# Kernel tuning notes

Measured on AMD Instinct MI355X. Metric: run time of the kernel, lower is better.

The kernel has to match this reference:

```python
import jax, jax.numpy as jnp
import numpy as np

N_SP, N_SPAT = 20000, 10000
E_SS, E_BIP, E_SP = 160000, 320000, 320000
H, C = 4, 64  # GAT heads / per-head channels (hidden_channels=64, concat=False)
EPS = 1e-6


def _gat(xs, xd, row, col, ea, Ws, Wd, a_s, a_d, a_e, We, b, num_dst, heads, ch, self_loops, concat):
    # PyG GATConv with edge_dim: linear -> per-head additive attention -> softmax over incoming edges -> scatter-add
    hs = (xs @ Ws).reshape(-1, heads, ch)          # [Ns,H,C]
    hd = (xd @ Wd).reshape(-1, heads, ch)          # [Nd,H,C]
    al_s = jnp.sum(hs * a_s, -1)                   # [Ns,H]
    al_d = jnp.sum(hd * a_d, -1)                   # [Nd,H]
    if self_loops:
        # add_self_loops with fill_value='mean': loop edge_attr = mean of incoming edge_attr per node
        cnt = jax.ops.segment_sum(jnp.ones((row.shape[0],), ea.dtype), col, num_dst)
        loop_ea = jax.ops.segment_sum(ea, col, num_dst) / jnp.maximum(cnt, 1.0)[:, None]
        loops = jnp.arange(num_dst, dtype=row.dtype)
        row = jnp.concatenate([row, loops])
        col = jnp.concatenate([col, loops])
        ea = jnp.concatenate([ea, loop_ea], 0)
    he = (ea @ We).reshape(-1, heads, ch)          # [E,H,C]
    al = jax.nn.leaky_relu(al_s[row] + al_d[col] + jnp.sum(he * a_e, -1), 0.2)  # [E,H]
    m = jax.ops.segment_max(al, col, num_segments=num_dst)
    ex = jnp.exp(al - m[col])
    den = jax.ops.segment_sum(ex, col, num_segments=num_dst)
    alpha = ex / (den[col] + 1e-16)
    out = jax.ops.segment_sum(hs[row] * alpha[..., None], col, num_segments=num_dst)  # [Nd,H,C]
    out = out.reshape(num_dst, heads * ch) if concat else out.mean(1)
    return out + b


def setup_inputs() -> dict:
    key = jax.random.key(0)
    ks = iter(jax.random.split(key, 64))
    f = lambda shape: jax.random.normal(next(ks), shape, jnp.float32)
    w = lambda shape: f(shape) / np.sqrt(shape[0])
    inp = {}
    inp['species_x_mean'] = f((N_SP, 32))
    inp['species_x_std'] = jax.random.uniform(next(ks), (N_SP, 32), jnp.float32)
    inp['traits_nanmask'] = jax.random.bernoulli(next(ks), 0.4, (N_SP, 32))
    inp['species_x_gen'] = f((N_SP, 64))
    inp['species_x_phylo'] = f((N_SP, 128))
    inp['spatial_x'] = f((N_SPAT, 12))
    inp['spatial_global_data'] = f((N_SPAT, 4))
    ei = lambda e, ns, nd: jnp.stack([jax.random.randint(next(ks), (e,), 0, ns, jnp.int32),
                                      jax.random.randint(next(ks), (e,), 0, nd, jnp.int32)])
    inp['ss_edge_index'] = ei(E_SS, N_SPAT, N_SPAT)
    inp['ss_edge_attr'] = jax.random.uniform(next(ks), (E_SS, 1), jnp.float32)
    inp['bip_edge_index'] = ei(E_BIP, N_SPAT, N_SP)
    inp['bip_edge_attr'] = jax.random.uniform(next(ks), (E_BIP, 1), jnp.float32)
    inp['sp_edge_index'] = ei(E_SP, N_SP, N_SP)
    inp['sp_edge_attr'] = jax.random.uniform(next(ks), (E_SP, 1), jnp.float32)
    # GAT conv params: space_gnn (sg0, sg1), species_gnn (pg0, pg1)
    for nm, din in [('sg0', 16), ('sg1', 64), ('pg0', 128), ('pg1', 64)]:
        inp[nm + '_W'] = w((din, H * C))
        inp[nm + '_as'] = f((H, C)) * 0.1
        inp[nm + '_ad'] = f((H, C)) * 0.1
        inp[nm + '_ae'] = f((H, C)) * 0.1
        inp[nm + '_We'] = w((1, H * C))
        inp[nm + '_b'] = jnp.zeros((C,), jnp.float32)
    # bipartite GATConv: heads=1, concat=True, src dim=hidden=64, dst dim=in_gen+in_phylo=192
    inp['bp_Ws'] = w((64, 64))
    inp['bp_Wd'] = w((192, 64))
    inp['bp_as'] = f((1, 64)) * 0.1
    inp['bp_ad'] = f((1, 64)) * 0.1
    inp['bp_ae'] = f((1, 64)) * 0.1
    inp['bp_We'] = w((1, 64))
    inp['bp_b'] = jnp.zeros((64,), jnp.float32)
    inp['sl_W'] = w((288, 64))
    inp['sl_b'] = jnp.zeros((64,), jnp.float32)
    inp['fc_W'] = w((64, 64))
    inp['fc_b'] = jnp.zeros((64,), jnp.float32)
    return inp


def reference(species_x_mean, species_x_std, traits_nanmask, species_x_gen, species_x_phylo,
              spatial_x, spatial_global_data, ss_edge_index, ss_edge_attr, bip_edge_index,
              bip_edge_attr, sp_edge_index, sp_edge_attr,
              sg0_W, sg0_as, sg0_ad, sg0_ae, sg0_We, sg0_b,
              sg1_W, sg1_as, sg1_ad, sg1_ae, sg1_We, sg1_b,
              pg0_W, pg0_as, pg0_ad, pg0_ae, pg0_We, pg0_b,
              pg1_W, pg1_as, pg1_ad, pg1_ae, pg1_We, pg1_b,
              bp_Ws, bp_Wd, bp_as, bp_ad, bp_ae, bp_We, bp_b,
              sl_W, sl_b, fc_W, fc_b):
    # inference path: no trait masking -> visibility = observed mask
    vis = (~traits_nanmask).astype(jnp.float32)
    sp_in = jnp.concatenate([species_x_mean, species_x_std, vis, species_x_gen, species_x_phylo], 1)
    sp_in = jax.nn.relu(sp_in @ sl_W + sl_b)                      # [N_SP,64]
    # spatial GNN (2 GATConv layers, heads=4, concat=False, self loops)
    h = jnp.concatenate([spatial_x, spatial_global_data], 1)      # [N_SPAT,16]
    r, c = ss_edge_index[0], ss_edge_index[1]
    h = jax.nn.relu(_gat(h, h, r, c, ss_edge_attr, sg0_W, sg0_W, sg0_as, sg0_ad, sg0_ae, sg0_We, sg0_b, N_SPAT, H, C, True, False))
    h = jax.nn.relu(_gat(h, h, r, c, ss_edge_attr, sg1_W, sg1_W, sg1_as, sg1_ad, sg1_ae, sg1_We, sg1_b, N_SPAT, H, C, True, False))
    # bipartite spatial->species GATConv (heads=1, concat=True, no self loops)
    part = jnp.concatenate([species_x_gen, species_x_phylo], 1)   # [N_SP,192]
    br, bc = bip_edge_index[0], bip_edge_index[1]
    sts = jax.nn.relu(_gat(h, part, br, bc, bip_edge_attr, bp_Ws, bp_Wd, bp_as, bp_ad, bp_ae, bp_We, bp_b, N_SP, 1, 64, False, True))
    # species GNN (2 GATConv layers)
    x = jnp.concatenate([sts, sp_in], 1)                          # [N_SP,128]
    pr, pc = sp_edge_index[0], sp_edge_index[1]
    x = jax.nn.relu(_gat(x, x, pr, pc, sp_edge_attr, pg0_W, pg0_W, pg0_as, pg0_ad, pg0_ae, pg0_We, pg0_b, N_SP, H, C, True, False))
    x = jax.nn.relu(_gat(x, x, pr, pc, sp_edge_attr, pg1_W, pg1_W, pg1_as, pg1_ad, pg1_ae, pg1_We, pg1_b, N_SP, H, C, True, False))
    ms = x @ fc_W + fc_b                                          # [N_SP, 2*out]
    mean, log_std = jnp.split(ms, 2, axis=-1)
    std = jax.nn.softplus(log_std) + EPS
    return mean, std
```

## Files before the change

kernel.cpp:

```cpp
#include <hip/hip_runtime.h>
#include <hip/hip_bf16.h>

#define NSP   20000
#define NSPAT 10000
#define ESS   160000
#define EBIP  320000
#define ESP   320000

static inline int cdiv_host(long a, long b) { return (int)((a + b - 1) / b); }

__device__ __forceinline__ float wave_red_sum(float p) {
#pragma unroll
  for (int m = 32; m >= 1; m >>= 1) p += __shfl_xor(p, m, 64);
  return p;
}
__device__ __forceinline__ float bf2f(unsigned short u) {
  return __uint_as_float(((unsigned int)u) << 16);
}
__device__ __forceinline__ unsigned short f2bf(float f) {
  unsigned int u = __float_as_uint(f);
  unsigned int r = (u + 0x7FFF + ((u >> 16) & 1)) >> 16;
  return (unsigned short)r;
}

__global__ void count3_kernel(
    const int* c1, int E1, int* cp1, int* rnk1, int n1,
    const int* c2, int E2, int* cp2, int* rnk2, int n2,
    const int* c3, int E3, int* cp3, int* rnk3, int n3,
    const unsigned int* __restrict__ mask, int* __restrict__ flag) {
  int b = blockIdx.x, t = threadIdx.x;
  if (b == gridDim.x - 1) {
    if (t < 64) {
      unsigned int w0 = mask[t], w1 = mask[t + 64], w2 = mask[t + 128], w3 = mask[t + 192];
      bool ai = (w0 <= 1u) && (w1 <= 1u) && (w2 <= 1u) && (w3 <= 1u);
      auto okf = [](unsigned int w) { return w == 0u || w == 0x3f800000u; };
      bool af = okf(w0) && okf(w1) && okf(w2) && okf(w3);
      unsigned long long bi = __ballot(ai), bf = __ballot(af);
      if (t == 0) *flag = (bi == ~0ull) ? 0 : ((bf == ~0ull) ? 2 : 1);
    }
    return;
  }
  int i = b * 256 + t;
  int total = E1 + E2 + E3;
  if (i >= total) return;
  int p = (i >> 8) & 7;
  if (i < E1) {
    int d = c1[i]; rnk1[i] = atomicAdd(&cp1[d * 8 + p], 1);
  } else if (i < E1 + E2) {
    int j = i - E1;
    int d = c2[j]; rnk2[j] = atomicAdd(&cp2[d * 8 + p], 1);
  } else {
    int j = i - E1 - E2;
    int d = c3[j]; rnk3[j] = atomicAdd(&cp3[d * 8 + p], 1);
  }
}

__global__ __launch_bounds__(1024) void mergescan3_kernel(
    int* cpA, int nA, int* ptrA,
    int* cpB, int nB, int* ptrB,
    int* cpC, int nC, int* ptrC) {
  int* cp; int n; int* ptr;
  if (blockIdx.x == 0) { cp = cpA; n = nA; ptr = ptrA; }
  else if (blockIdx.x == 1) { cp = cpB; n = nB; ptr = ptrB; }
  else { cp = cpC; n = nC; ptr = ptrC; }
  __shared__ int part[1024];
  int t = threadIdx.x;
  int ch = (n + 1023) / 1024;
  int beg = t * ch, end = min(beg + ch, n);
  int s = 0;
  for (int d = beg; d < end; ++d) {
#pragma unroll
    for (int p = 0; p < 8; ++p) s += cp[d * 8 + p];
  }
  part[t] = s;
  __syncthreads();
  for (int off = 1; off < 1024; off <<= 1) {
    int v = (t >= off) ? part[t - off] : 0;
    __syncthreads();
    part[t] += v;
    __syncthreads();
  }
  int run = (t == 0) ? 0 : part[t - 1];
  for (int d = beg; d < end; ++d) {
    ptr[d] = run;
    int acc = 0;
#pragma unroll
    for (int p = 0; p < 8; ++p) { int v = cp[d * 8 + p]; cp[d * 8 + p] = acc; acc += v; }
    run += acc;
  }
  if (t == 1023) ptr[n] = part[1023];
}

struct DoteArgs { const float* We[5]; const float* ae[5]; float* dotes; };
struct PrepArgs {
  const float* mean; const float* stdv; const void* mask; const int* flag;
  const float* sx; const float* sg; float* spc96; float* h0;
};

__global__ void scatter3x_kernel(
    const int* r1, const int* c1, const float* e1, int E1, const int* p1, const int* cp1, const int* k1, int n1, int* s1, float* a1,
    const int* r2, const int* c2, const float* e2, int E2, const int* p2, const int* cp2, const int* k2, int n2, int* s2, float* a2,
    const int* r3, const int* c3, const float* e3, int E3, const int* p3, const int* cp3, const int* k3, int n3, int* s3, float* a3,
    DoteArgs da, PrepArgs pa) {
  const int NB_SC = (ESS + EBIP + ESP + 255) / 256;
  int b = blockIdx.x, t = threadIdx.x;
  if (b < NB_SC) {
    int i = b * 256 + t;
    if (i >= E1 + E2 + E3) return;
    int p = (i >> 8) & 7;
    if (i < E1) {
      int d = c1[i];
      int pos = p1[d] + cp1[d * 8 + p] + k1[i];
      s1[pos] = r1[i]; a1[pos] = e1[i];
    } else if (i < E1 + E2) {
      int j = i - E1;
      int d = c2[j];
      int pos = p2[d] + cp2[d * 8 + p] + k2[j];
      s2[pos] = r2[j]; a2[pos] = e2[j];
    } else {
      int j = i - E1 - E2;
      int d = c3[j];
      int pos = p3[d] + cp3[d * 8 + p] + k3[j];
      s3[pos] = r3[j]; a3[pos] = e3[j];
    }
  } else if (b < NB_SC + 5) {
    int lb = b - NB_SC;
    int n = (lb == 2) ? 64 : 256;
    if (t < n) {
      float p = wave_red_sum(da.We[lb][t] * da.ae[lb][t]);
      if ((t & 63) == 0) da.dotes[lb * 4 + (t >> 6)] = p;
    }
  } else {
    const long totA = (long)NSP * 96;
    const long totB = (long)NSPAT * 16;
    long i = (long)(b - NB_SC - 5) * 256 + t;
    if (i >= totA + totB) return;
    int mode = *pa.flag;
    if (i < totA) {
      int n = (int)(i / 96), c = (int)(i % 96);
      float v;
      if (c < 32) v = pa.mean[(long)n * 32 + c];
      else if (c < 64) v = pa.stdv[(long)n * 32 + (c - 32)];
      else {
        long j = (long)n * 32 + (c - 64);
        int mv;
        if (mode == 0) mv = ((const int*)pa.mask)[j];
        else if (mode == 2) mv = (((const float*)pa.mask)[j] != 0.0f);
        else mv = (int)((const unsigned char*)pa.mask)[j];
        v = mv ? 0.f : 1.f;
      }
      pa.spc96[i] = v;
    } else {
      long k = i - totA;
      int n = (int)(k / 16), c = (int)(k % 16);
      pa.h0[k] = (c < 12) ? pa.sx[(long)n * 12 + c] : pa.sg[(long)n * 4 + (c - 12)];
    }
  }
}

struct XSrc { const float* p[5]; int w[5]; int n; };
struct PJob {
  XSrc xs; int M, K;
  const float* W; const float* bias; int mode;
  const float* a_s; const float* a_d;
  float* al_s; float* al_d;
  float* Y; float* Y2;
};
struct LeafArgs {
  const int* ss_ptr; const float* ss_cea; float* ss_lea;
  const int* pp_ptr; const float* pp_cea; float* pp_lea;
};

__device__ __forceinline__ void proj64_body(const PJob& J, int bid,
                                            float* wl, float* xl) {
  constexpr int KC = 32;
  constexpr int BR = 32;
  constexpr int KCP = 36;
  int t = threadIdx.x;
  long row0 = (long)bid * BR;
  if (row0 >= J.M) return;
  int cg = t & 15, rg = t >> 4;
  int c0 = cg * 4;

  float acc[2][4];
#pragma unroll
  for (int r = 0; r < 2; ++r)
#pragma unroll
    for (int j = 0; j < 4; ++j) acc[r][j] = 0.f;

  for (int k0 = 0; k0 < J.K; k0 += KC) {
    int seg = 0; int base = 0;
    while (k0 >= base + J.xs.w[seg]) { base += J.xs.w[seg]; ++seg; }
    const float* Xp = J.xs.p[seg];
    int stride = J.xs.w[seg];
    int kloc = k0 - base;

    __syncthreads();
    {
      const float4* ws = (const float4*)(J.W + (long)k0 * 64);
      float4* wd = (float4*)wl;
      wd[t] = ws[t];
      wd[t + 256] = ws[t + 256];
    }
    {
      int r = t >> 3, kq = (t & 7) * 4;
      long rr = row0 + r; if (rr >= J.M) rr = J.M - 1;
      float4 v = *(const float4*)(Xp + rr * stride + kloc + kq);
      *(float4*)(xl + r * KCP + kq) = v;
    }
    __syncthreads();

    for (int kg = 0; kg < KC; kg += 4) {
      float4 w0 = *(const float4*)(wl + (kg + 0) * 64 + c0);
      float4 w1 = *(const float4*)(wl + (kg + 1) * 64 + c0);
      float4 w2 = *(const float4*)(wl + (kg + 2) * 64 + c0);
      float4 w3 = *(const float4*)(wl + (kg + 3) * 64 + c0);
#pragma unroll
      for (int r = 0; r < 2; ++r) {
        float4 xv = *(const float4*)(xl + (rg * 2 + r) * KCP + kg);
        acc[r][0] = fmaf(xv.x, w0.x, acc[r][0]);
        acc[r][1] = fmaf(xv.x, w0.y, acc[r][1]);
        acc[r][2] = fmaf(xv.x, w0.z, acc[r][2]);
        acc[r][3] = fmaf(xv.x, w0.w, acc[r][3]);
        acc[r][0] = fmaf(xv.y, w1.x, acc[r][0]);
        acc[r][1] = fmaf(xv.y, w1.y, acc[r][1]);
        acc[r][2] = fmaf(xv.y, w1.z, acc[r][2]);
        acc[r][3] = fmaf(xv.y, w1.w, acc[r][3]);
        acc[r][0] = fmaf(xv.z, w2.x, acc[r][0]);
        acc[r][1] = fmaf(xv.z, w2.y, acc[r][1]);
        acc[r][2] = fmaf(xv.z, w2.z, acc[r][2]);
        acc[r][3] = fmaf(xv.z, w2.w, acc[r][3]);
        acc[r][0] = fmaf(xv.w, w3.x, acc[r][0]);
        acc[r][1] = fmaf(xv.w, w3.y, acc[r][1]);
        acc[r][2] = fmaf(xv.w, w3.z, acc[r][2]);
        acc[r][3] = fmaf(xv.w, w3.w, acc[r][3]);
      }
    }
  }

  float4 bv = make_float4(0.f, 0.f, 0.f, 0.f);
  float4 asv = make_float4(0.f, 0.f, 0.f, 0.f);
  float4 adv = make_float4(0.f, 0.f, 0.f, 0.f);
  if (J.bias) bv = *(const float4*)(J.bias + c0);
  if (J.a_s) asv = *(const float4*)(J.a_s + c0);
  if (J.a_d) adv = *(const float4*)(J.a_d + c0);

#pragma unroll
  for (int r = 0; r < 2; ++r) {
    long m = row0 + rg * 2 + r;
    bool ok = m < J.M;
    float v0 = acc[r][0] + bv.x, v1 = acc[r][1] + bv.y;
    float v2 = acc[r][2] + bv.z, v3 = acc[r][3] + bv.w;
    if (J.mode == 1) {
      if (ok)
        *(float4*)(J.Y + m * 64 + c0) = make_float4(
            fmaxf(v0, 0.f), fmaxf(v1, 0.f), fmaxf(v2, 0.f), fmaxf(v3, 0.f));
    } else if (J.mode == 2) {
      if (ok) {
        if (c0 < 32) {
          *(float4*)(J.Y + m * 32 + c0) = make_float4(v0, v1, v2, v3);
        } else {
          float4 o;
          o.x = fmaxf(v0, 0.f) + log1pf(__expf(-fabsf(v0))) + 1e-6f;
          o.y = fmaxf(v1, 0.f) + log1pf(__expf(-fabsf(v1))) + 1e-6f;
          o.z = fmaxf(v2, 0.f) + log1pf(__expf(-fabsf(v2))) + 1e-6f;
          o.w = fmaxf(v3, 0.f) + log1pf(__expf(-fabsf(v3))) + 1e-6f;
          *(float4*)(J.Y2 + m * 32 + (c0 - 32)) = o;
        }
      }
    } else if (ok && J.Y) {
      *(float4*)(J.Y + m * 64 + c0) = make_float4(v0, v1, v2, v3);
    }
    if (J.a_s) {
      float s = acc[r][0] * asv.x + acc[r][1] * asv.y + acc[r][2] * asv.z + acc[r][3] * asv.w;
      s += __shfl_xor(s, 1); s += __shfl_xor(s, 2);
      s += __shfl_xor(s, 4); s += __shfl_xor(s, 8);
      if (ok && cg == 0) J.al_s[m] = s;
    }
    if (J.a_d) {
      float s = acc[r][0] * adv.x + acc[r][1] * adv.y + acc[r][2] * adv.z + acc[r][3] * adv.w;
      s += __shfl_xor(s, 1); s += __shfl_xor(s, 2);
      s += __shfl_xor(s, 4); s += __shfl_xor(s, 8);
      if (ok && cg == 0) J.al_d[m] = s;
    }
  }
}

__global__ __launch_bounds__(256) void proj64x2l_kernel(PJob j0, PJob j1,
                                                        int nb0, int nb1,
                                                        LeafArgs la) {
  __shared__ float wl[32 * 64];
  __shared__ float xl[32 * 36];
  int b = blockIdx.x, t = threadIdx.x;
  if (b < nb0) {
    proj64_body(j0, b, wl, xl);
  } else if (b < nb0 + nb1) {
    proj64_body(j1, b - nb0, wl, xl);
  } else {
    int i = (b - nb0 - nb1) * 256 + t;
    if (i >= NSPAT + NSP) return;
    const int* ptr; const float* cea; float* lea; int d;
    if (i < NSPAT) { ptr = la.ss_ptr; cea = la.ss_cea; lea = la.ss_lea; d = i; }
    else { ptr = la.pp_ptr; cea = la.pp_cea; lea = la.pp_lea; d = i - NSPAT; }
    int e0 = ptr[d], e1 = ptr[d + 1];
    float s = 0.f;
    for (int e = e0; e < e1; ++e) s += cea[e];
    lea[d] = s / (float)max(e1 - e0, 1);
  }
}

__global__ __launch_bounds__(256) void proj_kernel(
    XSrc xsrc, int M, int K,
    const float* __restrict__ W,
    const float* __restrict__ a_s, const float* __restrict__ a_d,
    float* __restrict__ al_s, float* __restrict__ al_d,
    unsigned short* __restrict__ Y) {
  constexpr int KC = 32;
  constexpr int RPT = 8;
  constexpr int BR = 32;
  constexpr int KCP = 36;
  constexpr int H = 4;
  __shared__ float wl[KC * 256];
  __shared__ float xl[BR * KCP];

  int t = threadIdx.x;
  int cg = t & 63, rg = t >> 6;
  int c0 = cg * 4;
  long row0 = (long)blockIdx.x * BR;

  float acc[RPT][4];
#pragma unroll
  for (int r = 0; r < RPT; ++r)
#pragma unroll
    for (int j = 0; j < 4; ++j) acc[r][j] = 0.f;

  for (int k0 = 0; k0 < K; k0 += KC) {
    int kc = min(KC, K - k0);
    int seg = 0; int base = 0;
    while (k0 >= base + xsrc.w[seg]) { base += xsrc.w[seg]; ++seg; }
    const float* Xp = xsrc.p[seg];
    int stride = xsrc.w[seg];
    int kloc = k0 - base;

    __syncthreads();
    {
      const float4* wsrc = (const float4*)(W + (long)k0 * 256);
      float4* wdst = (float4*)wl;
      for (int i = t; i < (kc * 256) >> 2; i += 256) wdst[i] = wsrc[i];
    }
    for (int i = t; i < BR * 8; i += 256) {
      int r = i >> 3, kq = (i & 7) * 4;
      if (kq < kc) {
        long rr = row0 + r; if (rr >= M) rr = M - 1;
        float4 v = *(const float4*)(Xp + rr * stride + kloc + kq);
        *(float4*)(xl + r * KCP + kq) = v;
      }
    }
    __syncthreads();

    for (int kg = 0; kg < kc; kg += 4) {
      float4 w0 = *(const float4*)(wl + (kg + 0) * 256 + c0);
      float4 w1 = *(const float4*)(wl + (kg + 1) * 256 + c0);
      float4 w2 = *(const float4*)(wl + (kg + 2) * 256 + c0);
      float4 w3 = *(const float4*)(wl + (kg + 3) * 256 + c0);
      float4 xv[RPT];
#pragma unroll
      for (int r = 0; r < RPT; ++r)
        xv[r] = *(const float4*)(xl + (rg * RPT + r) * KCP + kg);
#pragma unroll
      for (int r = 0; r < RPT; ++r) {
        acc[r][0] = fmaf(xv[r].x, w0.x, acc[r][0]);
        acc[r][1] = fmaf(xv[r].x, w0.y, acc[r][1]);
        acc[r][2] = fmaf(xv[r].x, w0.z, acc[r][2]);
        acc[r][3] = fmaf(xv[r].x, w0.w, acc[r][3]);
        acc[r][0] = fmaf(xv[r].y, w1.x, acc[r][0]);
        acc[r][1] = fmaf(xv[r].y, w1.y, acc[r][1]);
        acc[r][2] = fmaf(xv[r].y, w1.z, acc[r][2]);
        acc[r][3] = fmaf(xv[r].y, w1.w, acc[r][3]);
        acc[r][0] = fmaf(xv[r].z, w2.x, acc[r][0]);
        acc[r][1] = fmaf(xv[r].z, w2.y, acc[r][1]);
        acc[r][2] = fmaf(xv[r].z, w2.z, acc[r][2]);
        acc[r][3] = fmaf(xv[r].z, w2.w, acc[r][3]);
        acc[r][0] = fmaf(xv[r].w, w3.x, acc[r][0]);
        acc[r][1] = fmaf(xv[r].w, w3.y, acc[r][1]);
        acc[r][2] = fmaf(xv[r].w, w3.z, acc[r][2]);
        acc[r][3] = fmaf(xv[r].w, w3.w, acc[r][3]);
      }
    }
  }

  float4 asv = *(const float4*)(a_s + c0);
  float4 adv = *(const float4*)(a_d + c0);

#pragma unroll
  for (int r = 0; r < RPT; ++r) {
    long m = row0 + (long)rg * RPT + r;
    bool ok = m < M;
    if (ok) {
      ushort4 o;
      o.x = f2bf(acc[r][0]); o.y = f2bf(acc[r][1]);
      o.z = f2bf(acc[r][2]); o.w = f2bf(acc[r][3]);
      *(ushort4*)(Y + m * 256 + c0) = o;
    }
    float s = acc[r][0] * asv.x + acc[r][1] * asv.y + acc[r][2] * asv.z + acc[r][3] * asv.w;
    s += __shfl_xor(s, 1); s += __shfl_xor(s, 2);
    s += __shfl_xor(s, 4); s += __shfl_xor(s, 8);
    if (ok && (cg & 15) == 0) al_s[m * H + (c0 >> 6)] = s;
    float d = acc[r][0] * adv.x + acc[r][1] * adv.y + acc[r][2] * adv.z + acc[r][3] * adv.w;
    d += __shfl_xor(d, 1); d += __shfl_xor(d, 2);
    d += __shfl_xor(d, 4); d += __shfl_xor(d, 8);
    if (ok && (cg & 15) == 0) al_d[m * H + (c0 >> 6)] = d;
  }
}

__device__ __forceinline__ void fma4_bf(float4& a, float al, ushort4 u) {
  a.x = fmaf(al, bf2f(u.x), a.x); a.y = fmaf(al, bf2f(u.y), a.y);
  a.z = fmaf(al, bf2f(u.z), a.z); a.w = fmaf(al, bf2f(u.w), a.w);
}
__device__ __forceinline__ void scale4(float4& a, float s) {
  a.x *= s; a.y *= s; a.z *= s; a.w *= s;
}

struct OS4 { float m, d; float4 a; };
__device__ __forceinline__ void os4_init(OS4& o) {
  o.m = -INFINITY; o.d = 0.f; o.a = make_float4(0.f, 0.f, 0.f, 0.f);
}
__device__ __forceinline__ void os4_upd(OS4& o, float l, ushort4 u) {
  if (l > o.m) { float sc = __expf(o.m - l); o.d *= sc; scale4(o.a, sc); o.m = l; }
  float ex = __expf(l - o.m);
  o.d += ex; fma4_bf(o.a, ex, u);
}
__device__ __forceinline__ void os4_mrg(OS4& A, const OS4& B) {
  if (B.m == -INFINITY) return;
  if (A.m == -INFINITY) { A = B; return; }
  float M = fmaxf(A.m, B.m);
  float sA = __expf(A.m - M), sB = __expf(B.m - M);
  A.d = A.d * sA + B.d * sB;
  A.a.x = A.a.x * sA + B.a.x * sB;
  A.a.y = A.a.y * sA + B.a.y * sB;
  A.a.z = A.a.z * sA + B.a.z * sB;
  A.a.w = A.a.w * sA + B.a.w * sB;
  A.m = M;
}

template <bool SELFLOOP>
__device__ __forceinline__ float4 gat4_body(
    int n, int lane, const int* __restrict__ dptr, const int* __restrict__ csr_src,
    const float* __restrict__ csr_ea, const float* __restrict__ al_s,
    const float* __restrict__ al_d, const float* __restrict__ dote,
    const float* __restrict__ loop_ea, const unsigned short* __restrict__ hs) {
  int h = lane >> 4;
  float ald = al_d[(long)n * 4 + h];
  float de = dote[h];
  int e0 = dptr[n], e1 = dptr[n + 1];
  OS4 o0, o1, o2, o3;
  os4_init(o0); os4_init(o1); os4_init(o2); os4_init(o3);
  if (SELFLOOP) {
    float l = al_s[(long)n * 4 + h] + ald + loop_ea[n] * de;
    l = (l > 0.f) ? l : 0.2f * l;
    o0.m = l; o0.d = 1.f;
    ushort4 u = *(const ushort4*)(hs + (long)n * 256 + lane * 4);
    o0.a.x = bf2f(u.x); o0.a.y = bf2f(u.y); o0.a.z = bf2f(u.z); o0.a.w = bf2f(u.w);
  }
  int e = e0;
  for (; e + 4 <= e1; e += 4) {
    int s0 = csr_src[e], s1 = csr_src[e + 1], s2 = csr_src[e + 2], s3 = csr_src[e + 3];
    float l0 = al_s[(long)s0 * 4 + h] + ald + csr_ea[e] * de;
    float l1 = al_s[(long)s1 * 4 + h] + ald + csr_ea[e + 1] * de;
    float l2 = al_s[(long)s2 * 4 + h] + ald + csr_ea[e + 2] * de;
    float l3 = al_s[(long)s3 * 4 + h] + ald + csr_ea[e + 3] * de;
    ushort4 u0 = *(const ushort4*)(hs + (long)s0 * 256 + lane * 4);
    ushort4 u1 = *(const ushort4*)(hs + (long)s1 * 256 + lane * 4);
    ushort4 u2 = *(const ushort4*)(hs + (long)s2 * 256 + lane * 4);
    ushort4 u3 = *(const ushort4*)(hs + (long)s3 * 256 + lane * 4);
    l0 = (l0 > 0.f) ? l0 : 0.2f * l0;
    l1 = (l1 > 0.f) ? l1 : 0.2f * l1;
    l2 = (l2 > 0.f) ? l2 : 0.2f * l2;
    l3 = (l3 > 0.f) ? l3 : 0.2f * l3;
    os4_upd(o0, l0, u0); os4_upd(o1, l1, u1);
    os4_upd(o2, l2, u2); os4_upd(o3, l3, u3);
  }
  for (; e < e1; ++e) {
    int s0 = csr_src[e];
    float l0 = al_s[(long)s0 * 4 + h] + ald + csr_ea[e] * de;
    l0 = (l0 > 0.f) ? l0 : 0.2f * l0;
    ushort4 u0 = *(const ushort4*)(hs + (long)s0 * 256 + lane * 4);
    os4_upd(o0, l0, u0);
  }
  os4_mrg(o0, o1); os4_mrg(o2, o3); os4_mrg(o0, o2);
  float inv = 1.f / (o0.d + 1e-16f);
  scale4(o0.a, inv);
  float4 a0 = o0.a;
  a0.x += __shfl_xor(a0.x, 16); a0.y += __shfl_xor(a0.y, 16);
  a0.z += __shfl_xor(a0.z, 16); a0.w += __shfl_xor(a0.w, 16);
  a0.x += __shfl_xor(a0.x, 32); a0.y += __shfl_xor(a0.y, 32);
  a0.z += __shfl_xor(a0.z, 32); a0.w += __shfl_xor(a0.w, 32);
  return a0;
}

template <bool SELFLOOP>
__global__ __launch_bounds__(256) void gat4_fused(
    int Nd, const int* __restrict__ dptr, const int* __restrict__ csr_src,
    const float* __restrict__ csr_ea, const float* __restrict__ al_s,
    const float* __restrict__ al_d, const float* __restrict__ dote,
    const float* __restrict__ loop_ea, const unsigned short* __restrict__ hs,
    const float* __restrict__ bias, float* __restrict__ out) {
  int wave = threadIdx.x >> 6, lane = threadIdx.x & 63;
  int n = blockIdx.x * 4 + wave;
  if (n >= Nd) return;
  float4 a0 = gat4_body<SELFLOOP>(n, lane, dptr, csr_src, csr_ea, al_s, al_d,
                                  dote, loop_ea, hs);
  if (lane < 16) {
    float4 b = *(const float4*)(bias + lane * 4);
    float4 o;
    o.x = fmaxf(a0.x * 0.25f + b.x, 0.f);
    o.y = fmaxf(a0.y * 0.25f + b.y, 0.f);
    o.z = fmaxf(a0.z * 0.25f + b.z, 0.f);
    o.w = fmaxf(a0.w * 0.25f + b.w, 0.f);
    *(float4*)(out + (long)n * 64 + lane * 4) = o;
  }
}

__global__ __launch_bounds__(256) void gat4_fc(
    int Nd, const int* __restrict__ dptr, const int* __restrict__ csr_src,
    const float* __restrict__ csr_ea, const float* __restrict__ al_s,
    const float* __restrict__ al_d, const float* __restrict__ dote,
    const float* __restrict__ loop_ea, const unsigned short* __restrict__ hs,
    const float* __restrict__ bias, const float* __restrict__ fcW,
    const float* __restrict__ fcb, float* __restrict__ meanO,
    float* __restrict__ stdO) {
  __shared__ float Wl[64 * 64];
  int t = threadIdx.x;
  {
    const float4* ws = (const float4*)fcW;
    float4* wd = (float4*)Wl;
    wd[t] = ws[t]; wd[t + 256] = ws[t + 256];
    wd[t + 512] = ws[t + 512]; wd[t + 768] = ws[t + 768];
  }
  __syncthreads();
  int wave = t >> 6, lane = t & 63;
  int n = blockIdx.x * 4 + wave;
  if (n >= Nd) return;
  float4 a0 = gat4_body<true>(n, lane, dptr, csr_src, csr_ea, al_s, al_d,
                              dote, loop_ea, hs);
  float4 b = *(const float4*)(bias + (lane & 15) * 4);
  float4 o;
  o.x = fmaxf(a0.x * 0.25f + b.x, 0.f);
  o.y = fmaxf(a0.y * 0.25f + b.y, 0.f);
  o.z = fmaxf(a0.z * 0.25f + b.z, 0.f);
  o.w = fmaxf(a0.w * 0.25f + b.w, 0.f);
  float accf = 0.f;
#pragma unroll
  for (int q = 0; q < 16; ++q) {
    float vx = __shfl(o.x, q), vy = __shfl(o.y, q);
    float vz = __shfl(o.z, q), vw = __shfl(o.w, q);
    accf = fmaf(vx, Wl[(4 * q + 0) * 64 + lane], accf);
    accf = fmaf(vy, Wl[(4 * q + 1) * 64 + lane], accf);
    accf = fmaf(vz, Wl[(4 * q + 2) * 64 + lane], accf);
    accf = fmaf(vw, Wl[(4 * q + 3) * 64 + lane], accf);
  }
  float v = accf + fcb[lane];
  if (lane < 32) {
    meanO[(long)n * 32 + lane] = v;
  } else {
    stdO[(long)n * 32 + (lane - 32)] =
        fmaxf(v, 0.f) + log1pf(__expf(-fabsf(v))) + 1e-6f;
  }
}

__device__ __forceinline__ void os1_upd(float& m, float& d, float& c, float l, float hv) {
  if (l > m) { float sc = __expf(m - l); d *= sc; c *= sc; m = l; }
  float ex = __expf(l - m);
  d += ex; c = fmaf(ex, hv, c);
}
__device__ __forceinline__ void os1_mrg(float& m0, float& d0, float& c0,
                                        float m1, float d1, float c1) {
  if (m1 == -INFINITY) return;
  if (m0 == -INFINITY) { m0 = m1; d0 = d1; c0 = c1; return; }
  float M = fmaxf(m0, m1);
  float sA = __expf(m0 - M), sB = __expf(m1 - M);
  d0 = d0 * sA + d1 * sB; c0 = c0 * sA + c1 * sB; m0 = M;
}

__global__ __launch_bounds__(256) void gat1_fused(
    int Nd, const int* __restrict__ dptr, const int* __restrict__ csr_src,
    const float* __restrict__ csr_ea, const float* __restrict__ al_s,
    const float* __restrict__ al_d, const float* __restrict__ dote,
    const float* __restrict__ hs, const float* __restrict__ bias,
    float* __restrict__ out) {
  int wave = threadIdx.x >> 6, lane = threadIdx.x & 63;
  int n = blockIdx.x * 4 + wave;
  if (n >= Nd) return;
  float ald = al_d[n];
  float de = dote[0];
  int e0 = dptr[n], e1 = dptr[n + 1];
  float m0 = -INFINITY, d0 = 0.f, c0 = 0.f;
  float m1 = -INFINITY, d1 = 0.f, c1 = 0.f;
  float m2 = -INFINITY, d2 = 0.f, c2 = 0.f;
  float m3 = -INFINITY, d3 = 0.f, c3 = 0.f;
  int e = e0;
  for (; e + 4 <= e1; e += 4) {
    int s0 = csr_src[e], s1 = csr_src[e + 1], s2 = csr_src[e + 2], s3 = csr_src[e + 3];
    float l0 = al_s[s0] + ald + csr_ea[e] * de;
    float l1 = al_s[s1] + ald + csr_ea[e + 1] * de;
    float l2 = al_s[s2] + ald + csr_ea[e + 2] * de;
    float l3 = al_s[s3] + ald + csr_ea[e + 3] * de;
    float h0 = hs[(long)s0 * 64 + lane];
    float h1 = hs[(long)s1 * 64 + lane];
    float h2 = hs[(long)s2 * 64 + lane];
    float h3 = hs[(long)s3 * 64 + lane];
    l0 = (l0 > 0.f) ? l0 : 0.2f * l0;
    l1 = (l1 > 0.f) ? l1 : 0.2f * l1;
    l2 = (l2 > 0.f) ? l2 : 0.2f * l2;
    l3 = (l3 > 0.f) ? l3 : 0.2f * l3;
    os1_upd(m0, d0, c0, l0, h0); os1_upd(m1, d1, c1, l1, h1);
    os1_upd(m2, d2, c2, l2, h2); os1_upd(m3, d3, c3, l3, h3);
  }
  for (; e < e1; ++e) {
    int s0 = csr_src[e];
    float l0 = al_s[s0] + ald + csr_ea[e] * de;
    l0 = (l0 > 0.f) ? l0 : 0.2f * l0;
    float h0 = hs[(long)s0 * 64 + lane];
    os1_upd(m0, d0, c0, l0, h0);
  }
  os1_mrg(m0, d0, c0, m1, d1, c1);
  os1_mrg(m2, d2, c2, m3, d3, c3);
  os1_mrg(m0, d0, c0, m2, d2, c2);
  float o = c0 / (d0 + 1e-16f);
  out[(long)n * 64 + lane] = fmaxf(o + bias[lane], 0.f);
}

extern "C" void kernel_launch(void* const* d_in, const int* in_sizes, int n_in,
                              void* d_out, int out_size, void* d_ws, size_t ws_size,
                              hipStream_t stream) {
  const float* sp_mean = (const float*)d_in[0];
  const float* sp_std  = (const float*)d_in[1];
  const void*  nanmask = d_in[2];
  const float* sp_gen  = (const float*)d_in[3];
  const float* sp_phy  = (const float*)d_in[4];
  const float* spat_x  = (const float*)d_in[5];
  const float* spat_g  = (const float*)d_in[6];
  const int*   ss_ei   = (const int*)d_in[7];
  const float* ss_ea   = (const float*)d_in[8];
  const int*   bip_ei  = (const int*)d_in[9];
  const float* bip_ea  = (const float*)d_in[10];
  const int*   sp_ei   = (const int*)d_in[11];
  const float* sp_ea   = (const float*)d_in[12];
  const float* sg0_W = (const float*)d_in[13]; const float* sg0_as = (const float*)d_in[14];
  const float* sg0_ad = (const float*)d_in[15]; const float* sg0_ae = (const float*)d_in[16];
  const float* sg0_We = (const float*)d_in[17]; const float* sg0_b = (const float*)d_in[18];
  const float* sg1_W = (const float*)d_in[19]; const float* sg1_as = (const float*)d_in[20];
  const float* sg1_ad = (const float*)d_in[21]; const float* sg1_ae = (const float*)d_in[22];
  const float* sg1_We = (const float*)d_in[23]; const float* sg1_b = (const float*)d_in[24];
  const float* pg0_W = (const float*)d_in[25]; const float* pg0_as = (const float*)d_in[26];
  const float* pg0_ad = (const float*)d_in[27]; const float* pg0_ae = (const float*)d_in[28];
  const float* pg0_We = (const float*)d_in[29]; const float* pg0_b = (const float*)d_in[30];
  const float* pg1_W = (const float*)d_in[31]; const float* pg1_as = (const float*)d_in[32];
  const float* pg1_ad = (const float*)d_in[33]; const float* pg1_ae = (const float*)d_in[34];
  const float* pg1_We = (const float*)d_in[35]; const float* pg1_b = (const float*)d_in[36];
  const float* bp_Ws = (const float*)d_in[37]; const float* bp_Wd = (const float*)d_in[38];
  const float* bp_as = (const float*)d_in[39]; const float* bp_ad = (const float*)d_in[40];
  const float* bp_ae = (const float*)d_in[41]; const float* bp_We = (const float*)d_in[42];
  const float* bp_b  = (const float*)d_in[43];
  const float* sl_W  = (const float*)d_in[44]; const float* sl_b  = (const float*)d_in[45];
  const float* fc_W  = (const float*)d_in[46]; const float* fc_b  = (const float*)d_in[47];

  char* wsb = (char*)d_ws;
  size_t off = 0;
  auto A = [&](size_t nbytes) -> void* {
    void* p = wsb + off;
    off += (nbytes + 255) & ~(size_t)255;
    return p;
  };
  int* ss_cp = (int*)A((size_t)8 * NSPAT * 4);
  int* bp_cp = (int*)A((size_t)8 * NSP * 4);
  int* pp_cp = (int*)A((size_t)8 * NSP * 4);
  size_t zbytes = off;
  int*   flag  = (int*)A(4);
  float* dotes = (float*)A(5 * 4 * sizeof(float));
  float* alS   = (float*)A((size_t)NSP * 4 * 4);
  float* alD   = (float*)A((size_t)NSP * 4 * 4);
  float* alSb  = (float*)A((size_t)NSPAT * 4);
  float* alDb  = (float*)A((size_t)NSP * 4);
  float* spc96 = (float*)A((size_t)NSP * 96 * 4);
  float* sp_in = (float*)A((size_t)NSP * 64 * 4);
  float* h0    = (float*)A((size_t)NSPAT * 16 * 4);
  float* h_a   = (float*)A((size_t)NSPAT * 64 * 4);
  float* h_b   = (float*)A((size_t)NSPAT * 64 * 4);
  float* HS    = (float*)A((size_t)NSP * 256 * 4);
  float* sts   = (float*)A((size_t)NSP * 64 * 4);
  float* x1    = (float*)A((size_t)NSP * 64 * 4);
  int*   ss_ptr = (int*)A((NSPAT + 1) * 4);
  int*   ss_src = (int*)A((size_t)ESS * 4);
  float* ss_cea = (float*)A((size_t)ESS * 4);
  int*   ss_rnk = (int*)A((size_t)ESS * 4);
  float* ss_lea = (float*)A((size_t)NSPAT * 4);
  int*   bp_ptr = (int*)A((NSP + 1) * 4);
  int*   bp_src = (int*)A((size_t)EBIP * 4);
  float* bp_cea = (float*)A((size_t)EBIP * 4);
  int*   bp_rnk = (int*)A((size_t)EBIP * 4);
  int*   pp_ptr = (int*)A((NSP + 1) * 4);
  int*   pp_src = (int*)A((size_t)ESP * 4);
  float* pp_cea = (float*)A((size_t)ESP * 4);
  int*   pp_rnk = (int*)A((size_t)ESP * 4);
  float* pp_lea = (float*)A((size_t)NSP * 4);
  (void)ws_size; (void)in_sizes; (void)n_in; (void)out_size;

  const int TB = 256;
  hipMemsetAsync(wsb, 0, zbytes, stream);

  count3_kernel<<<cdiv_host(ESS + EBIP + ESP, TB) + 1, TB, 0, stream>>>(
      ss_ei + ESS, ESS, ss_cp, ss_rnk, NSPAT,
      bip_ei + EBIP, EBIP, bp_cp, bp_rnk, NSP,
      sp_ei + ESP, ESP, pp_cp, pp_rnk, NSP,
      (const unsigned int*)nanmask, flag);
  mergescan3_kernel<<<3, 1024, 0, stream>>>(ss_cp, NSPAT, ss_ptr,
                                            bp_cp, NSP, bp_ptr,
                                            pp_cp, NSP, pp_ptr);

  {
    DoteArgs da{};
    da.We[0] = sg0_We; da.ae[0] = sg0_ae;
    da.We[1] = sg1_We; da.ae[1] = sg1_ae;
    da.We[2] = bp_We;  da.ae[2] = bp_ae;
    da.We[3] = pg0_We; da.ae[3] = pg0_ae;
    da.We[4] = pg1_We; da.ae[4] = pg1_ae;
    da.dotes = dotes;
    PrepArgs pa{ sp_mean, sp_std, nanmask, flag, spat_x, spat_g, spc96, h0 };
    int nb = cdiv_host(ESS + EBIP + ESP, TB) + 5 +
             cdiv_host((long)NSP * 96 + (long)NSPAT * 16, TB);
    scatter3x_kernel<<<nb, TB, 0, stream>>>(
        ss_ei, ss_ei + ESS, ss_ea, ESS, ss_ptr, ss_cp, ss_rnk, NSPAT, ss_src, ss_cea,
        bip_ei, bip_ei + EBIP, bip_ea, EBIP, bp_ptr, bp_cp, bp_rnk, NSP, bp_src, bp_cea,
        sp_ei, sp_ei + ESP, sp_ea, ESP, pp_ptr, pp_cp, pp_rnk, NSP, pp_src, pp_cea,
        da, pa);
  }

  {
    PJob j0{}; j0.xs.p[0] = spc96; j0.xs.w[0] = 96; j0.xs.p[1] = sp_gen; j0.xs.w[1] = 64;
    j0.xs.p[2] = sp_phy; j0.xs.w[2] = 128; j0.xs.n = 3;
    j0.M = NSP; j0.K = 288; j0.W = sl_W; j0.bias = sl_b; j0.mode = 1; j0.Y = sp_in;
    PJob j1{}; j1.xs.p[0] = sp_gen; j1.xs.w[0] = 64; j1.xs.p[1] = sp_phy; j1.xs.w[1] = 128;
    j1.xs.n = 2;
    j1.M = NSP; j1.K = 192; j1.W = bp_Wd; j1.mode = 0; j1.a_d = bp_ad; j1.al_d = alDb;
    LeafArgs la{ ss_ptr, ss_cea, ss_lea, pp_ptr, pp_cea, pp_lea };
    int nb0 = cdiv_host(NSP, 32), nb1 = cdiv_host(NSP, 32);
    int nbl = cdiv_host(NSPAT + NSP, TB);
    proj64x2l_kernel<<<nb0 + nb1 + nbl, TB, 0, stream>>>(j0, j1, nb0, nb1, la);
  }

  {
    XSrc xs{}; xs.p[0] = h0; xs.w[0] = 16; xs.n = 1;
    proj_kernel<<<cdiv_host(NSPAT, 32), TB, 0, stream>>>(xs, NSPAT, 16, sg0_W,
        sg0_as, sg0_ad, alS, alD, (unsigned short*)HS);
  }
  gat4_fused<true><<<cdiv_host(NSPAT, 4), TB, 0, stream>>>(
      NSPAT, ss_ptr, ss_src, ss_cea, alS, alD, dotes + 0, ss_lea,
      (const unsigned short*)HS, sg0_b, h_a);
  {
    XSrc xs{}; xs.p[0] = h_a; xs.w[0] = 64; xs.n = 1;
    proj_kernel<<<cdiv_host(NSPAT, 32), TB, 0, stream>>>(xs, NSPAT, 64, sg1_W,
        sg1_as, sg1_ad, alS, alD, (unsigned short*)HS);
  }
  gat4_fused<true><<<cdiv_host(NSPAT, 4), TB, 0, stream>>>(
      NSPAT, ss_ptr, ss_src, ss_cea, alS, alD, dotes + 4, ss_lea,
      (const unsigned short*)HS, sg1_b, h_b);

  {
    PJob j0{}; j0.xs.p[0] = h_b; j0.xs.w[0] = 64; j0.xs.n = 1;
    j0.M = NSPAT; j0.K = 64; j0.W = bp_Ws; j0.mode = 0;
    j0.a_s = bp_as; j0.al_s = alSb; j0.Y = h_a;
    LeafArgs la{ ss_ptr, ss_cea, ss_lea, pp_ptr, pp_cea, pp_lea };
    int nb0 = cdiv_host(NSPAT, 32);
    proj64x2l_kernel<<<nb0, TB, 0, stream>>>(j0, j0, nb0, 0, la);
  }
  gat1_fused<<<cdiv_host(NSP, 4), TB, 0, stream>>>(
      NSP, bp_ptr, bp_src, bp_cea, alSb, alDb, dotes + 8, h_a, bp_b, sts);

  {
    XSrc xs{}; xs.p[0] = sts; xs.w[0] = 64; xs.p[1] = sp_in; xs.w[1] = 64; xs.n = 2;
    proj_kernel<<<cdiv_host(NSP, 32), TB, 0, stream>>>(xs, NSP, 128, pg0_W,
        pg0_as, pg0_ad, alS, alD, (unsigned short*)HS);
  }
  gat4_fused<true><<<cdiv_host(NSP, 4), TB, 0, stream>>>(
      NSP, pp_ptr, pp_src, pp_cea, alS, alD, dotes + 12, pp_lea,
      (const unsigned short*)HS, pg0_b, x1);
  {
    XSrc xs{}; xs.p[0] = x1; xs.w[0] = 64; xs.n = 1;
    proj_kernel<<<cdiv_host(NSP, 32), TB, 0, stream>>>(xs, NSP, 64, pg1_W,
        pg1_as, pg1_ad, alS, alD, (unsigned short*)HS);
  }
  gat4_fc<<<cdiv_host(NSP, 4), TB, 0, stream>>>(
      NSP, pp_ptr, pp_src, pp_cea, alS, alD, dotes + 16, pp_lea,
      (const unsigned short*)HS, pg1_b, fc_W, fc_b,
      (float*)d_out, (float*)d_out + (long)NSP * 32);
}
```

Measured before the change: 528.0 us.

## Transpose per-partition edge counters and split merge-scan into parallel merge plus scan

Changes the 8-way partitioned per-destination counters from [node][8] to [8][node] layout. The per-node prefix over the 8 partitions moves out of the 3-block scan into a fully parallel merge kernel that writes per-node totals. The 3-block scan then only scans one count array. This cuts the serial work done inside the few-block scan, but adds a kernel launch and an extra count buffer.

```diff
diff --git a/kernel.cpp b/kernel.cpp
--- a/kernel.cpp
+++ b/kernel.cpp
@@ -45,33 +45,46 @@
   if (i >= total) return;
   int p = (i >> 8) & 7;
   if (i < E1) {
-    int d = c1[i]; rnk1[i] = atomicAdd(&cp1[d * 8 + p], 1);
+    int d = c1[i]; rnk1[i] = atomicAdd(&cp1[p * n1 + d], 1);
   } else if (i < E1 + E2) {
     int j = i - E1;
-    int d = c2[j]; rnk2[j] = atomicAdd(&cp2[d * 8 + p], 1);
+    int d = c2[j]; rnk2[j] = atomicAdd(&cp2[p * n2 + d], 1);
   } else {
     int j = i - E1 - E2;
-    int d = c3[j]; rnk3[j] = atomicAdd(&cp3[d * 8 + p], 1);
-  }
-}
-
-__global__ __launch_bounds__(1024) void mergescan3_kernel(
-    int* cpA, int nA, int* ptrA,
-    int* cpB, int nB, int* ptrB,
-    int* cpC, int nC, int* ptrC) {
-  int* cp; int n; int* ptr;
-  if (blockIdx.x == 0) { cp = cpA; n = nA; ptr = ptrA; }
-  else if (blockIdx.x == 1) { cp = cpB; n = nB; ptr = ptrB; }
-  else { cp = cpC; n = nC; ptr = ptrC; }
+    int d = c3[j]; rnk3[j] = atomicAdd(&cp3[p * n3 + d], 1);
+  }
+}
+
+__global__ void merge3_kernel(int* cp1, int* c1, int n1,
+                              int* cp2, int* c2, int n2,
+                              int* cp3, int* c3, int n3) {
+  int i = blockIdx.x * blockDim.x + threadIdx.x;
+  int total = n1 + n2 + n3;
+  if (i >= total) return;
+  int *cp, *c; int n, d;
+  if (i < n1) { cp = cp1; c = c1; n = n1; d = i; }
+  else if (i < n1 + n2) { cp = cp2; c = c2; n = n2; d = i - n1; }
+  else { cp = cp3; c = c3; n = n3; d = i - n1 - n2; }
+  int s = 0;
+#pragma unroll
+  for (int p = 0; p < 8; ++p) { int t = cp[p * n + d]; cp[p * n + d] = s; s += t; }
+  c[d] = s;
+}
+
+__global__ __launch_bounds__(1024) void scan3_kernel(
+    const int* cntA, int nA, int* ptrA,
+    const int* cntB, int nB, int* ptrB,
+    const int* cntC, int nC, int* ptrC) {
+  const int* cnt; int n; int* ptr;
+  if (blockIdx.x == 0) { cnt = cntA; n = nA; ptr = ptrA; }
+  else if (blockIdx.x == 1) { cnt = cntB; n = nB; ptr = ptrB; }
+  else { cnt = cntC; n = nC; ptr = ptrC; }
   __shared__ int part[1024];
   int t = threadIdx.x;
   int ch = (n + 1023) / 1024;
   int beg = t * ch, end = min(beg + ch, n);
   int s = 0;
-  for (int d = beg; d < end; ++d) {
-#pragma unroll
-    for (int p = 0; p < 8; ++p) s += cp[d * 8 + p];
-  }
+  for (int i = beg; i < end; ++i) s += cnt[i];
   part[t] = s;
   __syncthreads();
   for (int off = 1; off < 1024; off <<= 1) {
@@ -81,13 +94,7 @@
     __syncthreads();
   }
   int run = (t == 0) ? 0 : part[t - 1];
-  for (int d = beg; d < end; ++d) {
-    ptr[d] = run;
-    int acc = 0;
-#pragma unroll
-    for (int p = 0; p < 8; ++p) { int v = cp[d * 8 + p]; cp[d * 8 + p] = acc; acc += v; }
-    run += acc;
-  }
+  for (int i = beg; i < end; ++i) { ptr[i] = run; run += cnt[i]; }
   if (t == 1023) ptr[n] = part[1023];
 }
 
@@ -110,17 +117,17 @@
     int p = (i >> 8) & 7;
     if (i < E1) {
       int d = c1[i];
-      int pos = p1[d] + cp1[d * 8 + p] + k1[i];
+      int pos = p1[d] + cp1[p * n1 + d] + k1[i];
       s1[pos] = r1[i]; a1[pos] = e1[i];
     } else if (i < E1 + E2) {
       int j = i - E1;
       int d = c2[j];
-      int pos = p2[d] + cp2[d * 8 + p] + k2[j];
+      int pos = p2[d] + cp2[p * n2 + d] + k2[j];
       s2[pos] = r2[j]; a2[pos] = e2[j];
     } else {
       int j = i - E1 - E2;
       int d = c3[j];
-      int pos = p3[d] + cp3[d * 8 + p] + k3[j];
+      int pos = p3[d] + cp3[p * n3 + d] + k3[j];
       s3[pos] = r3[j]; a3[pos] = e3[j];
     }
   } else if (b < NB_SC + 5) {
@@ -676,6 +683,9 @@
   int* bp_cp = (int*)A((size_t)8 * NSP * 4);
   int* pp_cp = (int*)A((size_t)8 * NSP * 4);
   size_t zbytes = off;
+  int*   ss_cnt = (int*)A((NSPAT + 1) * 4);
+  int*   bp_cnt = (int*)A((NSP + 1) * 4);
+  int*   pp_cnt = (int*)A((NSP + 1) * 4);
   int*   flag  = (int*)A(4);
   float* dotes = (float*)A(5 * 4 * sizeof(float));
   float* alS   = (float*)A((size_t)NSP * 4 * 4);
@@ -714,9 +724,9 @@
       bip_ei + EBIP, EBIP, bp_cp, bp_rnk, NSP,
       sp_ei + ESP, ESP, pp_cp, pp_rnk, NSP,
       (const unsigned int*)nanmask, flag);
-  mergescan3_kernel<<<3, 1024, 0, stream>>>(ss_cp, NSPAT, ss_ptr,
-                                            bp_cp, NSP, bp_ptr,
-                                            pp_cp, NSP, pp_ptr);
+  merge3_kernel<<<cdiv_host(NSPAT + NSP + NSP, TB), TB, 0, stream>>>(
+      ss_cp, ss_cnt, NSPAT, bp_cp, bp_cnt, NSP, pp_cp, pp_cnt, NSP);
+  scan3_kernel<<<3, 1024, 0, stream>>>(ss_cnt, NSPAT, ss_ptr, bp_cnt, NSP, bp_ptr, pp_cnt, NSP, pp_ptr);
 
   {
     DoteArgs da{};
```

Measured after the change: 473.3 us. 1.12x faster.
